# Kernel optimization log

Measured on AMD Instinct MI355X. Metric: run time of the kernel, lower is better.

## Reference

```python
import jax, jax.numpy as jnp
import numpy as np

D_MODEL = 1024
N_HEADS = 16
D_HEAD = D_MODEL // N_HEADS
EPS_LN = 1e-5
EPS_GATE = 1e-5
EPS_DEN = 1e-5


def setup_inputs() -> dict:
    key = jax.random.key(0)
    ks = jax.random.split(key, 4)
    B, T, D = 1, 2048, D_MODEL
    x = jax.random.normal(ks[0], (B, T, D), dtype=jnp.float32)
    # Linear weights scaled like torch default init (~1/sqrt(fan_in))
    s = 1.0 / np.sqrt(D)
    qkv_w = jax.random.normal(ks[1], (3 * D, D), dtype=jnp.float32) * s
    gate_w = jax.random.normal(ks[2], (D, D), dtype=jnp.float32) * s
    proj_w = jax.random.normal(ks[3], (D, D), dtype=jnp.float32) * s
    return {
        "x": x,
        "ln_g": jnp.ones((D,), jnp.float32),
        "ln_b": jnp.zeros((D,), jnp.float32),
        "qkv_w": qkv_w,
        "qkv_b": jnp.zeros((3 * D,), jnp.float32),
        "gate_w": gate_w,
        "gate_b": jnp.zeros((D,), jnp.float32),
        "proj_w": proj_w,
        "proj_b": jnp.zeros((D,), jnp.float32),
    }


def _linear(x, w, b):
    # torch nn.Linear: y = x @ W^T + b, W is (out, in)
    return jnp.einsum("btd,od->bto", x, w) + b


def reference(x, ln_g, ln_b, qkv_w, qkv_b, gate_w, gate_b, proj_w, proj_b):
    B, T, D = x.shape
    H, Dh = N_HEADS, D_HEAD

    # LayerNorm
    mu = jnp.mean(x, axis=-1, keepdims=True)
    var = jnp.mean((x - mu) ** 2, axis=-1, keepdims=True)
    x_norm = (x - mu) / jnp.sqrt(var + EPS_LN) * ln_g + ln_b

    qkv = _linear(x_norm, qkv_w, qkv_b)
    q, k, v = jnp.split(qkv, 3, axis=-1)

    # concept gate on raw x
    gate_sig = jax.nn.sigmoid(_linear(x, gate_w, gate_b))
    gate_norm = gate_sig / (jnp.mean(gate_sig, axis=-1, keepdims=True) + EPS_GATE)
    q = q * gate_norm
    k = k * gate_norm

    # (B,T,D) -> (B,H,T,Dh)
    def heads(t):
        return t.reshape(B, T, H, Dh).transpose(0, 2, 1, 3)

    q, k, v = heads(q).astype(jnp.float32), heads(k).astype(jnp.float32), heads(v).astype(jnp.float32)

    q = jax.nn.elu(q) + 1.0
    k = jax.nn.elu(k) + 1.0

    # causal linear attention via cumsum of outer products (same math as source)
    kv = jnp.einsum("bhtd,bhtm->bhtdm", k, v)        # (B,H,T,Dh,Dh)
    kv_cum = jnp.cumsum(kv, axis=2)
    out_num = jnp.einsum("bhtd,bhtdm->bhtm", q, kv_cum)
    k_cum = jnp.cumsum(k, axis=2)
    out_den = jnp.einsum("bhtd,bhtd->bht", q, k_cum)[..., None] + EPS_DEN
    out = out_num / out_den                           # (B,H,T,Dh)

    out = out.astype(x_norm.dtype).transpose(0, 2, 1, 3).reshape(B, T, D)
    return _linear(out, proj_w, proj_b)
```

## Files before the change

### kernel.cpp

```cpp
#include <hip/hip_runtime.h>
#include <hip/hip_bf16.h>
#include <math.h>

#define T_SEQ 2048
#define DM 1024
#define NH 16
#define DH 64
#define CHUNK 64
#define NCHUNK (T_SEQ / CHUNK)

typedef __hip_bfloat16 bf16;
typedef __attribute__((ext_vector_type(8))) short short8;
typedef __attribute__((ext_vector_type(4))) short short4v;
typedef __attribute__((ext_vector_type(4))) float f32x4;

static __device__ __forceinline__ short f2b_bits(float f) {
  bf16 t = __float2bfloat16(f);
  short s;
  __builtin_memcpy(&s, &t, 2);
  return s;
}

static __device__ __forceinline__ float gelu1(float raw, float gate, float inv) {
  float x = raw * gate * inv;
  return x > 0.f ? x + 1.f : __expf(x);
}

static __device__ __forceinline__ void gload16(const void* g, void* l) {
  __builtin_amdgcn_global_load_lds((const __attribute__((address_space(1))) void*)g,
                                   (__attribute__((address_space(3))) void*)l, 16, 0, 0);
}

__global__ __launch_bounds__(256) void f2b3_kernel(const float* __restrict__ qkv,
                                                   const float* __restrict__ gw,
                                                   const float* __restrict__ pw,
                                                   bf16* __restrict__ oq,
                                                   bf16* __restrict__ og,
                                                   bf16* __restrict__ op) {
  constexpr int NQ = 3 * DM * DM / 4, NS = DM * DM / 4;
  int i = blockIdx.x * 256 + threadIdx.x;
  const float* src;
  bf16* dst;
  int j;
  if (i < NQ) { src = qkv; dst = oq; j = i; }
  else if (i < NQ + NS) { src = gw; dst = og; j = i - NQ; }
  else if (i < NQ + 2 * NS) { src = pw; dst = op; j = i - NQ - NS; }
  else return;
  float4 v = ((const float4*)src)[j];
  short4v s;
  s.x = f2b_bits(v.x); s.y = f2b_bits(v.y); s.z = f2b_bits(v.z); s.w = f2b_bits(v.w);
  *(short4v*)&dst[j * 4] = s;
}

__global__ __launch_bounds__(256) void ln_kernel(const float* __restrict__ x,
                                                 const float* __restrict__ g,
                                                 const float* __restrict__ b,
                                                 bf16* __restrict__ xn,
                                                 bf16* __restrict__ xbf) {
  const int row = blockIdx.x;
  const float* xr = x + (size_t)row * DM;
  float vals[4];
  float s = 0.f, s2 = 0.f;
#pragma unroll
  for (int i = 0; i < 4; i++) {
    float v = xr[threadIdx.x + i * 256];
    vals[i] = v;
    s += v;
    s2 += v * v;
  }
#pragma unroll
  for (int m = 1; m < 64; m <<= 1) {
    s += __shfl_xor(s, m, 64);
    s2 += __shfl_xor(s2, m, 64);
  }
  __shared__ float red[8];
  const int wid = threadIdx.x >> 6;
  if ((threadIdx.x & 63) == 0) {
    red[wid] = s;
    red[4 + wid] = s2;
  }
  __syncthreads();
  s = red[0] + red[1] + red[2] + red[3];
  s2 = red[4] + red[5] + red[6] + red[7];
  const float mean = s * (1.f / DM);
  const float var = s2 * (1.f / DM) - mean * mean;
  const float rstd = rsqrtf(var + 1e-5f);
#pragma unroll
  for (int i = 0; i < 4; i++) {
    int idx = threadIdx.x + i * 256;
    float v = (vals[i] - mean) * rstd * g[idx] + b[idx];
    xn[(size_t)row * DM + idx] = __float2bfloat16(v);
    xbf[(size_t)row * DM + idx] = __float2bfloat16(vals[i]);
  }
}

__global__ __launch_bounds__(256) void gemm_gateqkv(
    const bf16* __restrict__ xbf, const bf16* __restrict__ xn,
    const bf16* __restrict__ wg, const bf16* __restrict__ wq,
    const float* __restrict__ gate_b, const float* __restrict__ qkv_b,
    float* __restrict__ gate_sig, float* __restrict__ Qraw,
    float* __restrict__ Kraw, float* __restrict__ Vo) {
  constexpr int K = 1024;
  __shared__ __align__(16) short As[2 * 128 * 32];
  __shared__ __align__(16) short Bs[2 * 128 * 32];

  const int tid = threadIdx.x;
  const int wid = tid >> 6, lane = tid & 63;
  const int wm = wid >> 1, wn = wid & 1;
  const int lm = lane & 15, quad = lane >> 4;

  const bool isGate = blockIdx.y < 8;
  const int m0 = blockIdx.x * 128;
  const int n0 = isGate ? blockIdx.y * 128 : (blockIdx.y - 8) * 128;
  const short* Ag = (const short*)(isGate ? xbf : xn);
  const short* Wg = (const short*)(isGate ? wg : wq);
  const float* bias = isGate ? gate_b : qkv_b;

  f32x4 zero = {0.f, 0.f, 0.f, 0.f};
  f32x4 acc[4][4];
#pragma unroll
  for (int i = 0; i < 4; i++)
#pragma unroll
    for (int j = 0; j < 4; j++) acc[i][j] = zero;

  for (int kb = 0; kb < K; kb += 64) {
    __syncthreads();
#pragma unroll
    for (int sec = 0; sec < 2; sec++) {
#pragma unroll
      for (int it = 0; it < 2; it++) {
        const int idx = it * 256 + tid;
        const int row = idx >> 2, seg = (idx & 3) * 8;
        gload16(&Ag[(size_t)(m0 + row) * K + kb + sec * 32 + seg],
                &As[sec * 4096 + (it * 256 + wid * 64) * 8]);
        gload16(&Wg[(size_t)(n0 + row) * K + kb + sec * 32 + seg],
                &Bs[sec * 4096 + (it * 256 + wid * 64) * 8]);
      }
    }
    __syncthreads();
#pragma unroll
    for (int sec = 0; sec < 2; sec++) {
      short8 afr[4], bfr[4];
#pragma unroll
      for (int i = 0; i < 4; i++) {
        afr[i] = *(const short8*)&As[sec * 4096 + (wm * 64 + i * 16 + lm) * 32 + quad * 8];
        bfr[i] = *(const short8*)&Bs[sec * 4096 + (wn * 64 + i * 16 + lm) * 32 + quad * 8];
      }
#pragma unroll
      for (int i = 0; i < 4; i++)
#pragma unroll
        for (int j = 0; j < 4; j++)
          acc[i][j] = __builtin_amdgcn_mfma_f32_16x16x32_bf16(afr[i], bfr[j], acc[i][j], 0, 0, 0);
    }
  }

#pragma unroll
  for (int i = 0; i < 4; i++) {
    const int rbase = m0 + wm * 64 + i * 16 + quad * 4;
#pragma unroll
    for (int j = 0; j < 4; j++) {
      const int col = n0 + wn * 64 + j * 16 + lm;
      const float bval = bias[col];
#pragma unroll
      for (int r = 0; r < 4; r++) {
        const int row = rbase + r;
        float v = acc[i][j][r] + bval;
        if (isGate) {
          gate_sig[(size_t)row * DM + col] = 1.f / (1.f + __expf(-v));
        } else if (col < DM) {
          const int d = col;
          Qraw[((size_t)(d >> 6) * T_SEQ + row) * DH + (d & 63)] = v;
        } else if (col < 2 * DM) {
          const int d = col - DM;
          Kraw[((size_t)(d >> 6) * T_SEQ + row) * DH + (d & 63)] = v;
        } else {
          const int d = col - 2 * DM;
          Vo[((size_t)(d >> 6) * T_SEQ + row) * DH + (d & 63)] = v;
        }
      }
    }
  }
}

__global__ __launch_bounds__(256) void gemm_proj(const bf16* __restrict__ A,
                                                 const bf16* __restrict__ W,
                                                 const float* __restrict__ bias,
                                                 float* __restrict__ Cout) {
  constexpr int K = 1024;
  __shared__ __align__(16) short As[2 * 64 * 32];
  __shared__ __align__(16) short Bs[2 * 128 * 32];

  const int tid = threadIdx.x;
  const int wid = tid >> 6, lane = tid & 63;
  const int wm = wid >> 1, wn = wid & 1;
  const int lm = lane & 15, quad = lane >> 4;

  const int m0 = blockIdx.x * 64;
  const int n0 = blockIdx.y * 128;
  const short* Ag = (const short*)A;
  const short* Wg = (const short*)W;

  f32x4 zero = {0.f, 0.f, 0.f, 0.f};
  f32x4 acc[2][4];
#pragma unroll
  for (int i = 0; i < 2; i++)
#pragma unroll
    for (int j = 0; j < 4; j++) acc[i][j] = zero;

  for (int kb = 0; kb < K; kb += 64) {
    __syncthreads();
#pragma unroll
    for (int sec = 0; sec < 2; sec++) {
      {
        const int row = tid >> 2, seg = (tid & 3) * 8;
        gload16(&Ag[(size_t)(m0 + row) * K + kb + sec * 32 + seg],
                &As[sec * 2048 + (wid * 64) * 8]);
      }
#pragma unroll
      for (int it = 0; it < 2; it++) {
        const int idx = it * 256 + tid;
        const int row = idx >> 2, seg = (idx & 3) * 8;
        gload16(&Wg[(size_t)(n0 + row) * K + kb + sec * 32 + seg],
                &Bs[sec * 4096 + (it * 256 + wid * 64) * 8]);
      }
    }
    __syncthreads();
#pragma unroll
    for (int sec = 0; sec < 2; sec++) {
      short8 afr[2], bfr[4];
#pragma unroll
      for (int i = 0; i < 2; i++)
        afr[i] = *(const short8*)&As[sec * 2048 + (wm * 32 + i * 16 + lm) * 32 + quad * 8];
#pragma unroll
      for (int j = 0; j < 4; j++)
        bfr[j] = *(const short8*)&Bs[sec * 4096 + (wn * 64 + j * 16 + lm) * 32 + quad * 8];
#pragma unroll
      for (int i = 0; i < 2; i++)
#pragma unroll
        for (int j = 0; j < 4; j++)
          acc[i][j] = __builtin_amdgcn_mfma_f32_16x16x32_bf16(afr[i], bfr[j], acc[i][j], 0, 0, 0);
    }
  }
#pragma unroll
  for (int i = 0; i < 2; i++) {
    const int rbase = m0 + wm * 32 + i * 16 + quad * 4;
#pragma unroll
    for (int j = 0; j < 4; j++) {
      const int col = n0 + wn * 64 + j * 16 + lm;
      const float bval = bias[col];
#pragma unroll
      for (int r = 0; r < 4; r++)
        Cout[(size_t)(rbase + r) * DM + col] = acc[i][j][r] + bval;
    }
  }
}

__global__ __launch_bounds__(256) void gate_mean_kernel(const float* __restrict__ gate_sig,
                                                        float* __restrict__ inv_den) {
  const int row = blockIdx.x;
  float s = 0.f;
  for (int i = threadIdx.x; i < DM; i += 256) s += gate_sig[(size_t)row * DM + i];
#pragma unroll
  for (int m = 1; m < 64; m <<= 1) s += __shfl_xor(s, m, 64);
  __shared__ float red[4];
  if ((threadIdx.x & 63) == 0) red[threadIdx.x >> 6] = s;
  __syncthreads();
  if (threadIdx.x == 0) {
    float tot = red[0] + red[1] + red[2] + red[3];
    inv_den[row] = 1.f / (tot * (1.f / DM) + 1e-5f);
  }
}

__global__ __launch_bounds__(256, 2) void chunk_sum_mm(const float* __restrict__ Kraw,
                                                       const float* __restrict__ gate_sig,
                                                       const float* __restrict__ inv_den,
                                                       const float* __restrict__ Vo,
                                                       float* __restrict__ Skv,
                                                       float* __restrict__ Sk) {
  constexpr int STR = 68;
  __shared__ __align__(16) float Ks2[64 * STR];
  __shared__ __align__(16) float Vs2[64 * STR];
  const int b = blockIdx.x;
  const int h = b >> 5, c = b & 31;
  const int tid = threadIdx.x;
  const int ty = tid >> 4, tx = tid & 15;
  const int d0 = ty * 4, m0 = tx * 4;
  const int t0 = c * CHUNK;
  const size_t cb = ((size_t)h * T_SEQ + t0) * DH;
  const float* Kg = Kraw + cb;
  const float* Vg = Vo + cb;
#pragma unroll
  for (int p = 0; p < 4; p++) {
    int f = p * 256 + tid, row = f >> 4, seg = (f & 15) * 4;
    const int t = t0 + row;
    f32x4 kr = *(const f32x4*)&Kg[row * 64 + seg];
    f32x4 gr = *(const f32x4*)&gate_sig[(size_t)t * DM + h * 64 + seg];
    const float inv = inv_den[t];
    f32x4 kgv;
#pragma unroll
    for (int e = 0; e < 4; e++) kgv[e] = gelu1(kr[e], gr[e], inv);
    *(f32x4*)&Ks2[row * STR + seg] = kgv;
    *(f32x4*)&Vs2[row * STR + seg] = *(const f32x4*)&Vg[row * 64 + seg];
  }
  __syncthreads();
  float acc[4][4] = {};
#pragma unroll 4
  for (int s = 0; s < 64; s++) {
    f32x4 kf = *(const f32x4*)&Ks2[s * STR + d0];
    f32x4 vf = *(const f32x4*)&Vs2[s * STR + m0];
#pragma unroll
    for (int i = 0; i < 4; i++)
#pragma unroll
      for (int j = 0; j < 4; j++) acc[i][j] += kf[i] * vf[j];
  }
  float* outp = Skv + (size_t)b * 4096;
#pragma unroll
  for (int i = 0; i < 4; i++) {
    f32x4 o = {acc[i][0], acc[i][1], acc[i][2], acc[i][3]};
    *(f32x4*)&outp[(d0 + i) * 64 + m0] = o;
  }
  if (tid < 64) {
    float ss = 0.f;
#pragma unroll 4
    for (int s = 0; s < 64; s++) ss += Ks2[s * STR + tid];
    Sk[b * 64 + tid] = ss;
  }
}

__global__ __launch_bounds__(256) void scan_excl(float* __restrict__ Skv,
                                                 float* __restrict__ Sk) {
  const int bid = blockIdx.x, tid = threadIdx.x;
  if (bid < 256) {
    const int id = bid * 256 + tid;
    const int h = id >> 12, e = id & 4095;
    float* base = Skv + (size_t)h * NCHUNK * 4096 + e;
    float v[NCHUNK];
#pragma unroll
    for (int c = 0; c < NCHUNK; c++) v[c] = base[(size_t)c * 4096];
    float run = 0.f;
#pragma unroll
    for (int c = 0; c < NCHUNK; c++) {
      float t = v[c];
      base[(size_t)c * 4096] = run;
      run += t;
    }
  } else {
    const int id = (bid - 256) * 256 + tid;
    const int h = id >> 6, e = id & 63;
    float* base = Sk + (size_t)h * NCHUNK * 64 + e;
    float v[NCHUNK];
#pragma unroll
    for (int c = 0; c < NCHUNK; c++) v[c] = base[c * 64];
    float run = 0.f;
#pragma unroll
    for (int c = 0; c < NCHUNK; c++) {
      float t = v[c];
      base[c * 64] = run;
      run += t;
    }
  }
}

__global__ __launch_bounds__(256, 2) void attn_mm(const float* __restrict__ Qraw,
                                                  const float* __restrict__ Kraw,
                                                  const float* __restrict__ gate_sig,
                                                  const float* __restrict__ inv_den,
                                                  const float* __restrict__ Vo,
                                                  const float* __restrict__ Skv,
                                                  const float* __restrict__ Sk,
                                                  bf16* __restrict__ O) {
  constexpr int STR = 68;
  __shared__ __align__(16) float Qs[64 * STR];
  __shared__ __align__(16) float Vs[64 * STR];
  __shared__ __align__(16) float KPs[64 * STR];
  __shared__ float denp[64 * 16];
  __shared__ float skp[64];
  __shared__ float den[64];
  const int b = blockIdx.x;
  const int h = b >> 5, c = b & 31;
  const int tid = threadIdx.x;
  const int ty = tid >> 4, tx = tid & 15;
  const int r0 = ty * 4, c0 = tx * 4, m0 = tx * 4;
  const int t0 = c * CHUNK;
  const size_t cb = ((size_t)h * T_SEQ + t0) * DH;
  const float* Qg = Qraw + cb;
  const float* Kg = Kraw + cb;
  const float* Vg = Vo + cb;
  const float* Pg = Skv + (size_t)b * 4096;

  f32x4 kreg[4], greg[4];
  float ireg[4];
#pragma unroll
  for (int p = 0; p < 4; p++) {
    int f = p * 256 + tid, row = f >> 4, seg = (f & 15) * 4;
    kreg[p] = *(const f32x4*)&Kg[row * 64 + seg];
    greg[p] = *(const f32x4*)&gate_sig[(size_t)(t0 + row) * DM + h * 64 + seg];
    ireg[p] = inv_den[t0 + row];
  }
#pragma unroll
  for (int p = 0; p < 4; p++) {
    int f = p * 256 + tid, row = f >> 4, seg = (f & 15) * 4;
    f32x4 qr = *(const f32x4*)&Qg[row * 64 + seg];
    f32x4 gq = *(const f32x4*)&gate_sig[(size_t)(t0 + row) * DM + h * 64 + seg];
    const float inv = inv_den[t0 + row];
    f32x4 qgv;
#pragma unroll
    for (int e = 0; e < 4; e++) qgv[e] = gelu1(qr[e], gq[e], inv);
    *(f32x4*)&Qs[row * STR + seg] = qgv;
    *(f32x4*)&Vs[row * STR + seg] = *(const f32x4*)&Vg[row * 64 + seg];
    *(f32x4*)&KPs[row * STR + seg] = *(const f32x4*)&Pg[row * 64 + seg];
  }
  if (tid < 64) skp[tid] = Sk[b * 64 + tid];
  __syncthreads();

  if (tid < 64) {
    float s = 1e-5f;
#pragma unroll 4
    for (int d = 0; d < 64; d++) s += Qs[tid * STR + d] * skp[d];
    den[tid] = s;
  }

  float accO[4][4] = {};
#pragma unroll 2
  for (int d0 = 0; d0 < 64; d0 += 4) {
    f32x4 qf[4], pf[4];
#pragma unroll
    for (int i = 0; i < 4; i++) qf[i] = *(const f32x4*)&Qs[(r0 + i) * STR + d0];
#pragma unroll
    for (int dd = 0; dd < 4; dd++) pf[dd] = *(const f32x4*)&KPs[(d0 + dd) * STR + m0];
#pragma unroll
    for (int i = 0; i < 4; i++)
#pragma unroll
      for (int j = 0; j < 4; j++)
        accO[i][j] += qf[i][0] * pf[0][j] + qf[i][1] * pf[1][j] +
                      qf[i][2] * pf[2][j] + qf[i][3] * pf[3][j];
  }
  __syncthreads();
#pragma unroll
  for (int p = 0; p < 4; p++) {
    int f = p * 256 + tid, row = f >> 4, seg = (f & 15) * 4;
    f32x4 kgv;
#pragma unroll
    for (int e = 0; e < 4; e++) kgv[e] = gelu1(kreg[p][e], greg[p][e], ireg[p]);
    *(f32x4*)&KPs[row * STR + seg] = kgv;
  }
  __syncthreads();

  float accS[4][4] = {};
#pragma unroll 2
  for (int d0 = 0; d0 < 64; d0 += 4) {
    f32x4 qf[4], kf[4];
#pragma unroll
    for (int i = 0; i < 4; i++) qf[i] = *(const f32x4*)&Qs[(r0 + i) * STR + d0];
#pragma unroll
    for (int j = 0; j < 4; j++) kf[j] = *(const f32x4*)&KPs[(c0 + j) * STR + d0];
#pragma unroll
    for (int i = 0; i < 4; i++)
#pragma unroll
      for (int j = 0; j < 4; j++)
        accS[i][j] += qf[i][0] * kf[j][0] + qf[i][1] * kf[j][1] +
                      qf[i][2] * kf[j][2] + qf[i][3] * kf[j][3];
  }
  float dp[4];
#pragma unroll
  for (int i = 0; i < 4; i++) {
    dp[i] = 0.f;
#pragma unroll
    for (int j = 0; j < 4; j++) {
      float v = (c0 + j) <= (r0 + i) ? accS[i][j] : 0.f;
      accS[i][j] = v;
      dp[i] += v;
    }
  }
  __syncthreads();
#pragma unroll
  for (int i = 0; i < 4; i++) {
    f32x4 sv = {accS[i][0], accS[i][1], accS[i][2], accS[i][3]};
    *(f32x4*)&Qs[(r0 + i) * STR + c0] = sv;
    denp[(r0 + i) * 16 + tx] = dp[i];
  }
  __syncthreads();
  if (tid < 64) {
    float s = den[tid];
#pragma unroll
    for (int t = 0; t < 16; t++) s += denp[tid * 16 + t];
    den[tid] = s;
  }

#pragma unroll 2
  for (int c4 = 0; c4 < 64; c4 += 4) {
    f32x4 sf[4], vf[4];
#pragma unroll
    for (int i = 0; i < 4; i++) sf[i] = *(const f32x4*)&Qs[(r0 + i) * STR + c4];
#pragma unroll
    for (int cc = 0; cc < 4; cc++) vf[cc] = *(const f32x4*)&Vs[(c4 + cc) * STR + m0];
#pragma unroll
    for (int i = 0; i < 4; i++)
#pragma unroll
      for (int j = 0; j < 4; j++)
        accO[i][j] += sf[i][0] * vf[0][j] + sf[i][1] * vf[1][j] +
                      sf[i][2] * vf[2][j] + sf[i][3] * vf[3][j];
  }
  __syncthreads();

#pragma unroll
  for (int i = 0; i < 4; i++) {
    const float inv = 1.f / den[r0 + i];
    short4v ov;
#pragma unroll
    for (int j = 0; j < 4; j++) ov[j] = f2b_bits(accO[i][j] * inv);
    *(short4v*)&O[(size_t)(t0 + r0 + i) * DM + h * 64 + m0] = ov;
  }
}

extern "C" void kernel_launch(void* const* d_in, const int* in_sizes, int n_in,
                              void* d_out, int out_size, void* d_ws, size_t ws_size,
                              hipStream_t stream) {
  (void)in_sizes; (void)n_in; (void)out_size; (void)ws_size;
  const float* x      = (const float*)d_in[0];
  const float* ln_g   = (const float*)d_in[1];
  const float* ln_b   = (const float*)d_in[2];
  const float* qkv_w  = (const float*)d_in[3];
  const float* qkv_b  = (const float*)d_in[4];
  const float* gate_w = (const float*)d_in[5];
  const float* gate_b = (const float*)d_in[6];
  const float* proj_w = (const float*)d_in[7];
  const float* proj_b = (const float*)d_in[8];
  float* out = (float*)d_out;

  char* ws = (char*)d_ws;
  size_t off = 0;
  auto alloc = [&](size_t bytes) {
    void* p = ws + off;
    off += (bytes + 255) & ~(size_t)255;
    return p;
  };
  bf16*  xn       = (bf16*)alloc((size_t)T_SEQ * DM * 2);
  bf16*  xbf      = (bf16*)alloc((size_t)T_SEQ * DM * 2);
  bf16*  wqkv     = (bf16*)alloc((size_t)3 * DM * DM * 2);
  bf16*  wgate    = (bf16*)alloc((size_t)DM * DM * 2);
  bf16*  wproj    = (bf16*)alloc((size_t)DM * DM * 2);
  float* gate_sig = (float*)alloc((size_t)T_SEQ * DM * 4);
  float* inv_den  = (float*)alloc((size_t)T_SEQ * 4);
  float* Qraw     = (float*)alloc((size_t)T_SEQ * DM * 4);
  float* Kraw     = (float*)alloc((size_t)T_SEQ * DM * 4);
  float* Vo       = (float*)alloc((size_t)T_SEQ * DM * 4);
  bf16*  Obuf     = (bf16*)alloc((size_t)T_SEQ * DM * 2);
  float* Skv      = (float*)alloc((size_t)NH * NCHUNK * 4096 * 4);
  float* Sk       = (float*)alloc((size_t)NH * NCHUNK * 64 * 4);

  const int n4_total = (3 + 1 + 1) * DM * DM / 4;
  f2b3_kernel<<<(n4_total + 255) / 256, 256, 0, stream>>>(qkv_w, gate_w, proj_w,
                                                          wqkv, wgate, wproj);
  ln_kernel<<<T_SEQ, 256, 0, stream>>>(x, ln_g, ln_b, xn, xbf);
  gemm_gateqkv<<<dim3(16, 32), 256, 0, stream>>>(xbf, xn, wgate, wqkv, gate_b, qkv_b,
                                                 gate_sig, Qraw, Kraw, Vo);
  gate_mean_kernel<<<T_SEQ, 256, 0, stream>>>(gate_sig, inv_den);
  chunk_sum_mm<<<NH * NCHUNK, 256, 0, stream>>>(Kraw, gate_sig, inv_den, Vo, Skv, Sk);
  scan_excl<<<260, 256, 0, stream>>>(Skv, Sk);
  attn_mm<<<NH * NCHUNK, 256, 0, stream>>>(Qraw, Kraw, gate_sig, inv_den, Vo, Skv, Sk, Obuf);
  gemm_proj<<<dim3(32, 8), 256, 0, stream>>>(Obuf, wproj, proj_b, out);
}
```

Baseline: 177.1 us.

## Fuse prep kernels, store QKV/gate as bf16, fold gate mean into GEMM epilogue

Merges the weight-conversion and layernorm kernels into one launch. The gate row-mean is now reduced in the gate GEMM epilogue through LDS and atomics, which removes the separate gate_mean kernel. Q, K, V and the gate sigmoid are stored as bf16 instead of fp32, halving the intermediate traffic for the chunk and attention kernels. In exchange it loses precision on the intermediates and makes the gate sum order nondeterministic because of the atomics.

```diff
diff --git a/kernel.cpp b/kernel.cpp
--- a/kernel.cpp
+++ b/kernel.cpp
@@ -20,6 +20,12 @@
   __builtin_memcpy(&s, &t, 2);
   return s;
 }
+static __device__ __forceinline__ float b2f(short s) {
+  unsigned int u = ((unsigned int)(unsigned short)s) << 16;
+  float f;
+  __builtin_memcpy(&f, &u, 4);
+  return f;
+}
 
 static __device__ __forceinline__ float gelu1(float raw, float gate, float inv) {
   float x = raw * gate * inv;
@@ -31,66 +37,65 @@
                                    (__attribute__((address_space(3))) void*)l, 16, 0, 0);
 }
 
-__global__ __launch_bounds__(256) void f2b3_kernel(const float* __restrict__ qkv,
-                                                   const float* __restrict__ gw,
-                                                   const float* __restrict__ pw,
-                                                   bf16* __restrict__ oq,
-                                                   bf16* __restrict__ og,
-                                                   bf16* __restrict__ op) {
-  constexpr int NQ = 3 * DM * DM / 4, NS = DM * DM / 4;
-  int i = blockIdx.x * 256 + threadIdx.x;
-  const float* src;
-  bf16* dst;
-  int j;
-  if (i < NQ) { src = qkv; dst = oq; j = i; }
-  else if (i < NQ + NS) { src = gw; dst = og; j = i - NQ; }
-  else if (i < NQ + 2 * NS) { src = pw; dst = op; j = i - NQ - NS; }
-  else return;
-  float4 v = ((const float4*)src)[j];
-  short4v s;
-  s.x = f2b_bits(v.x); s.y = f2b_bits(v.y); s.z = f2b_bits(v.z); s.w = f2b_bits(v.w);
-  *(short4v*)&dst[j * 4] = s;
-}
-
-__global__ __launch_bounds__(256) void ln_kernel(const float* __restrict__ x,
-                                                 const float* __restrict__ g,
-                                                 const float* __restrict__ b,
-                                                 bf16* __restrict__ xn,
-                                                 bf16* __restrict__ xbf) {
-  const int row = blockIdx.x;
-  const float* xr = x + (size_t)row * DM;
-  float vals[4];
-  float s = 0.f, s2 = 0.f;
-#pragma unroll
-  for (int i = 0; i < 4; i++) {
-    float v = xr[threadIdx.x + i * 256];
-    vals[i] = v;
-    s += v;
-    s2 += v * v;
-  }
-#pragma unroll
-  for (int m = 1; m < 64; m <<= 1) {
-    s += __shfl_xor(s, m, 64);
-    s2 += __shfl_xor(s2, m, 64);
-  }
-  __shared__ float red[8];
-  const int wid = threadIdx.x >> 6;
-  if ((threadIdx.x & 63) == 0) {
-    red[wid] = s;
-    red[4 + wid] = s2;
-  }
-  __syncthreads();
-  s = red[0] + red[1] + red[2] + red[3];
-  s2 = red[4] + red[5] + red[6] + red[7];
-  const float mean = s * (1.f / DM);
-  const float var = s2 * (1.f / DM) - mean * mean;
-  const float rstd = rsqrtf(var + 1e-5f);
-#pragma unroll
-  for (int i = 0; i < 4; i++) {
-    int idx = threadIdx.x + i * 256;
-    float v = (vals[i] - mean) * rstd * g[idx] + b[idx];
-    xn[(size_t)row * DM + idx] = __float2bfloat16(v);
-    xbf[(size_t)row * DM + idx] = __float2bfloat16(vals[i]);
+#define PREP_WBLOCKS (5 * DM * DM / 4 / 256)
+__global__ __launch_bounds__(256) void prep_kernel(
+    const float* __restrict__ x, const float* __restrict__ g,
+    const float* __restrict__ b, const float* __restrict__ qkv_w,
+    const float* __restrict__ gate_w, const float* __restrict__ proj_w,
+    bf16* __restrict__ xn, bf16* __restrict__ xbf,
+    bf16* __restrict__ wqkv, bf16* __restrict__ wgate, bf16* __restrict__ wproj,
+    float* __restrict__ gate_accum) {
+  const int blk = blockIdx.x;
+  if (blk < T_SEQ) {
+    const int row = blk;
+    if (row < 8) gate_accum[row * 256 + threadIdx.x] = 0.f;
+    const float* xr = x + (size_t)row * DM;
+    float vals[4];
+    float s = 0.f, s2 = 0.f;
+#pragma unroll
+    for (int i = 0; i < 4; i++) {
+      float v = xr[threadIdx.x + i * 256];
+      vals[i] = v;
+      s += v;
+      s2 += v * v;
+    }
+#pragma unroll
+    for (int m = 1; m < 64; m <<= 1) {
+      s += __shfl_xor(s, m, 64);
+      s2 += __shfl_xor(s2, m, 64);
+    }
+    __shared__ float red[8];
+    const int wid = threadIdx.x >> 6;
+    if ((threadIdx.x & 63) == 0) {
+      red[wid] = s;
+      red[4 + wid] = s2;
+    }
+    __syncthreads();
+    s = red[0] + red[1] + red[2] + red[3];
+    s2 = red[4] + red[5] + red[6] + red[7];
+    const float mean = s * (1.f / DM);
+    const float var = s2 * (1.f / DM) - mean * mean;
+    const float rstd = rsqrtf(var + 1e-5f);
+#pragma unroll
+    for (int i = 0; i < 4; i++) {
+      int idx = threadIdx.x + i * 256;
+      float v = (vals[i] - mean) * rstd * g[idx] + b[idx];
+      xn[(size_t)row * DM + idx] = __float2bfloat16(v);
+      xbf[(size_t)row * DM + idx] = __float2bfloat16(vals[i]);
+    }
+  } else {
+    constexpr int NQ = 3 * DM * DM / 4, NS = DM * DM / 4;
+    int i = (blk - T_SEQ) * 256 + threadIdx.x;
+    const float* src;
+    bf16* dst;
+    int j;
+    if (i < NQ) { src = qkv_w; dst = wqkv; j = i; }
+    else if (i < NQ + NS) { src = gate_w; dst = wgate; j = i - NQ; }
+    else { src = proj_w; dst = wproj; j = i - NQ - NS; }
+    float4 v = ((const float4*)src)[j];
+    short4v sv;
+    sv.x = f2b_bits(v.x); sv.y = f2b_bits(v.y); sv.z = f2b_bits(v.z); sv.w = f2b_bits(v.w);
+    *(short4v*)&dst[j * 4] = sv;
   }
 }
 
@@ -98,8 +103,8 @@
     const bf16* __restrict__ xbf, const bf16* __restrict__ xn,
     const bf16* __restrict__ wg, const bf16* __restrict__ wq,
     const float* __restrict__ gate_b, const float* __restrict__ qkv_b,
-    float* __restrict__ gate_sig, float* __restrict__ Qraw,
-    float* __restrict__ Kraw, float* __restrict__ Vo) {
+    short* __restrict__ Gb, float* __restrict__ gate_accum,
+    short* __restrict__ Qb, short* __restrict__ Kb, short* __restrict__ Vb) {
   constexpr int K = 1024;
   __shared__ __align__(16) short As[2 * 128 * 32];
   __shared__ __align__(16) short Bs[2 * 128 * 32];
@@ -114,7 +119,6 @@
   const int n0 = isGate ? blockIdx.y * 128 : (blockIdx.y - 8) * 128;
   const short* Ag = (const short*)(isGate ? xbf : xn);
   const short* Wg = (const short*)(isGate ? wg : wq);
-  const float* bias = isGate ? gate_b : qkv_b;
 
   f32x4 zero = {0.f, 0.f, 0.f, 0.f};
   f32x4 acc[4][4];
@@ -154,28 +158,56 @@
     }
   }
 
-#pragma unroll
-  for (int i = 0; i < 4; i++) {
-    const int rbase = m0 + wm * 64 + i * 16 + quad * 4;
-#pragma unroll
-    for (int j = 0; j < 4; j++) {
-      const int col = n0 + wn * 64 + j * 16 + lm;
-      const float bval = bias[col];
+  if (isGate) {
+    float* red = (float*)As;
+    __syncthreads();
+#pragma unroll
+    for (int i = 0; i < 4; i++) {
 #pragma unroll
       for (int r = 0; r < 4; r++) {
-        const int row = rbase + r;
-        float v = acc[i][j][r] + bval;
-        if (isGate) {
-          gate_sig[(size_t)row * DM + col] = 1.f / (1.f + __expf(-v));
-        } else if (col < DM) {
-          const int d = col;
-          Qraw[((size_t)(d >> 6) * T_SEQ + row) * DH + (d & 63)] = v;
-        } else if (col < 2 * DM) {
-          const int d = col - DM;
-          Kraw[((size_t)(d >> 6) * T_SEQ + row) * DH + (d & 63)] = v;
-        } else {
-          const int d = col - 2 * DM;
-          Vo[((size_t)(d >> 6) * T_SEQ + row) * DH + (d & 63)] = v;
+        const int rowl = wm * 64 + i * 16 + quad * 4 + r;
+        const int row = m0 + rowl;
+        float rp = 0.f;
+#pragma unroll
+        for (int j = 0; j < 4; j++) {
+          const int col = n0 + wn * 64 + j * 16 + lm;
+          float v = acc[i][j][r] + gate_b[col];
+          float sig = 1.f / (1.f + __expf(-v));
+          Gb[(size_t)row * DM + col] = f2b_bits(sig);
+          rp += sig;
+        }
+        red[rowl * 32 + wn * 16 + lm] = rp;
+      }
+    }
+    __syncthreads();
+    if (tid < 128) {
+      float s = 0.f;
+#pragma unroll
+      for (int t2 = 0; t2 < 32; t2++) s += red[tid * 32 + t2];
+      atomicAdd(&gate_accum[m0 + tid], s);
+    }
+  } else {
+#pragma unroll
+    for (int i = 0; i < 4; i++) {
+      const int rbase = m0 + wm * 64 + i * 16 + quad * 4;
+#pragma unroll
+      for (int j = 0; j < 4; j++) {
+        const int col = n0 + wn * 64 + j * 16 + lm;
+        const float bval = qkv_b[col];
+#pragma unroll
+        for (int r = 0; r < 4; r++) {
+          const int row = rbase + r;
+          const short bv = f2b_bits(acc[i][j][r] + bval);
+          if (col < DM) {
+            const int d = col;
+            Qb[((size_t)(d >> 6) * T_SEQ + row) * DH + (d & 63)] = bv;
+          } else if (col < 2 * DM) {
+            const int d = col - DM;
+            Kb[((size_t)(d >> 6) * T_SEQ + row) * DH + (d & 63)] = bv;
+          } else {
+            const int d = col - 2 * DM;
+            Vb[((size_t)(d >> 6) * T_SEQ + row) * DH + (d & 63)] = bv;
+          }
         }
       }
     }
@@ -255,26 +287,10 @@
   }
 }
 
-__global__ __launch_bounds__(256) void gate_mean_kernel(const float* __restrict__ gate_sig,
-                                                        float* __restrict__ inv_den) {
-  const int row = blockIdx.x;
-  float s = 0.f;
-  for (int i = threadIdx.x; i < DM; i += 256) s += gate_sig[(size_t)row * DM + i];
-#pragma unroll
-  for (int m = 1; m < 64; m <<= 1) s += __shfl_xor(s, m, 64);
-  __shared__ float red[4];
-  if ((threadIdx.x & 63) == 0) red[threadIdx.x >> 6] = s;
-  __syncthreads();
-  if (threadIdx.x == 0) {
-    float tot = red[0] + red[1] + red[2] + red[3];
-    inv_den[row] = 1.f / (tot * (1.f / DM) + 1e-5f);
-  }
-}
-
-__global__ __launch_bounds__(256, 2) void chunk_sum_mm(const float* __restrict__ Kraw,
-                                                       const float* __restrict__ gate_sig,
-                                                       const float* __restrict__ inv_den,
-                                                       const float* __restrict__ Vo,
+__global__ __launch_bounds__(256, 2) void chunk_sum_mm(const short* __restrict__ Kb,
+                                                       const short* __restrict__ Gb,
+                                                       const float* __restrict__ ga,
+                                                       const short* __restrict__ Vb,
                                                        float* __restrict__ Skv,
                                                        float* __restrict__ Sk) {
   constexpr int STR = 68;
@@ -287,20 +303,22 @@
   const int d0 = ty * 4, m0 = tx * 4;
   const int t0 = c * CHUNK;
   const size_t cb = ((size_t)h * T_SEQ + t0) * DH;
-  const float* Kg = Kraw + cb;
-  const float* Vg = Vo + cb;
 #pragma unroll
   for (int p = 0; p < 4; p++) {
     int f = p * 256 + tid, row = f >> 4, seg = (f & 15) * 4;
     const int t = t0 + row;
-    f32x4 kr = *(const f32x4*)&Kg[row * 64 + seg];
-    f32x4 gr = *(const f32x4*)&gate_sig[(size_t)t * DM + h * 64 + seg];
-    const float inv = inv_den[t];
-    f32x4 kgv;
-#pragma unroll
-    for (int e = 0; e < 4; e++) kgv[e] = gelu1(kr[e], gr[e], inv);
+    short4v kr = *(const short4v*)&Kb[cb + row * 64 + seg];
+    short4v gr = *(const short4v*)&Gb[(size_t)t * DM + h * 64 + seg];
+    short4v vr = *(const short4v*)&Vb[cb + row * 64 + seg];
+    const float inv = 1.f / (ga[t] * (1.f / DM) + 1e-5f);
+    f32x4 kgv, vv;
+#pragma unroll
+    for (int e = 0; e < 4; e++) {
+      kgv[e] = gelu1(b2f(kr[e]), b2f(gr[e]), inv);
+      vv[e] = b2f(vr[e]);
+    }
     *(f32x4*)&Ks2[row * STR + seg] = kgv;
-    *(f32x4*)&Vs2[row * STR + seg] = *(const f32x4*)&Vg[row * 64 + seg];
+    *(f32x4*)&Vs2[row * STR + seg] = vv;
   }
   __syncthreads();
   float acc[4][4] = {};
@@ -361,11 +379,11 @@
   }
 }
 
-__global__ __launch_bounds__(256, 2) void attn_mm(const float* __restrict__ Qraw,
-                                                  const float* __restrict__ Kraw,
-                                                  const float* __restrict__ gate_sig,
-                                                  const float* __restrict__ inv_den,
-                                                  const float* __restrict__ Vo,
+__global__ __launch_bounds__(256, 2) void attn_mm(const short* __restrict__ Qb,
+                                                  const short* __restrict__ Kb,
+                                                  const short* __restrict__ Gb,
+                                                  const float* __restrict__ ga,
+                                                  const short* __restrict__ Vb,
                                                   const float* __restrict__ Skv,
                                                   const float* __restrict__ Sk,
                                                   bf16* __restrict__ O) {
@@ -383,31 +401,32 @@
   const int r0 = ty * 4, c0 = tx * 4, m0 = tx * 4;
   const int t0 = c * CHUNK;
   const size_t cb = ((size_t)h * T_SEQ + t0) * DH;
-  const float* Qg = Qraw + cb;
-  const float* Kg = Kraw + cb;
-  const float* Vg = Vo + cb;
   const float* Pg = Skv + (size_t)b * 4096;
 
-  f32x4 kreg[4], greg[4];
+  short4v kreg[4], greg[4];
   float ireg[4];
 #pragma unroll
   for (int p = 0; p < 4; p++) {
     int f = p * 256 + tid, row = f >> 4, seg = (f & 15) * 4;
-    kreg[p] = *(const f32x4*)&Kg[row * 64 + seg];
-    greg[p] = *(const f32x4*)&gate_sig[(size_t)(t0 + row) * DM + h * 64 + seg];
-    ireg[p] = inv_den[t0 + row];
+    kreg[p] = *(const short4v*)&Kb[cb + row * 64 + seg];
+    greg[p] = *(const short4v*)&Gb[(size_t)(t0 + row) * DM + h * 64 + seg];
+    ireg[p] = 1.f / (ga[t0 + row] * (1.f / DM) + 1e-5f);
   }
 #pragma unroll
   for (int p = 0; p < 4; p++) {
     int f = p * 256 + tid, row = f >> 4, seg = (f & 15) * 4;
-    f32x4 qr = *(const f32x4*)&Qg[row * 64 + seg];
-    f32x4 gq = *(const f32x4*)&gate_sig[(size_t)(t0 + row) * DM + h * 64 + seg];
-    const float inv = inv_den[t0 + row];
-    f32x4 qgv;
-#pragma unroll
-    for (int e = 0; e < 4; e++) qgv[e] = gelu1(qr[e], gq[e], inv);
+    short4v qr = *(const short4v*)&Qb[cb + row * 64 + seg];
+    short4v gq = *(const short4v*)&Gb[(size_t)(t0 + row) * DM + h * 64 + seg];
+    short4v vr = *(const short4v*)&Vb[cb + row * 64 + seg];
+    const float inv = 1.f / (ga[t0 + row] * (1.f / DM) + 1e-5f);
+    f32x4 qgv, vv;
+#pragma unroll
+    for (int e = 0; e < 4; e++) {
+      qgv[e] = gelu1(b2f(qr[e]), b2f(gq[e]), inv);
+      vv[e] = b2f(vr[e]);
+    }
     *(f32x4*)&Qs[row * STR + seg] = qgv;
-    *(f32x4*)&Vs[row * STR + seg] = *(const f32x4*)&Vg[row * 64 + seg];
+    *(f32x4*)&Vs[row * STR + seg] = vv;
     *(f32x4*)&KPs[row * STR + seg] = *(const f32x4*)&Pg[row * 64 + seg];
   }
   if (tid < 64) skp[tid] = Sk[b * 64 + tid];
@@ -441,7 +460,7 @@
     int f = p * 256 + tid, row = f >> 4, seg = (f & 15) * 4;
     f32x4 kgv;
 #pragma unroll
-    for (int e = 0; e < 4; e++) kgv[e] = gelu1(kreg[p][e], greg[p][e], ireg[p]);
+    for (int e = 0; e < 4; e++) kgv[e] = gelu1(b2f(kreg[p][e]), b2f(greg[p][e]), ireg[p]);
     *(f32x4*)&KPs[row * STR + seg] = kgv;
   }
   __syncthreads();
@@ -540,24 +559,21 @@
   bf16*  wqkv     = (bf16*)alloc((size_t)3 * DM * DM * 2);
   bf16*  wgate    = (bf16*)alloc((size_t)DM * DM * 2);
   bf16*  wproj    = (bf16*)alloc((size_t)DM * DM * 2);
-  float* gate_sig = (float*)alloc((size_t)T_SEQ * DM * 4);
-  float* inv_den  = (float*)alloc((size_t)T_SEQ * 4);
-  float* Qraw     = (float*)alloc((size_t)T_SEQ * DM * 4);
-  float* Kraw     = (float*)alloc((size_t)T_SEQ * DM * 4);
-  float* Vo       = (float*)alloc((size_t)T_SEQ * DM * 4);
+  short* Gb       = (short*)alloc((size_t)T_SEQ * DM * 2);
+  float* gate_accum = (float*)alloc((size_t)T_SEQ * 4);
+  short* Qb       = (short*)alloc((size_t)T_SEQ * DM * 2);
+  short* Kb       = (short*)alloc((size_t)T_SEQ * DM * 2);
+  short* Vb       = (short*)alloc((size_t)T_SEQ * DM * 2);
   bf16*  Obuf     = (bf16*)alloc((size_t)T_SEQ * DM * 2);
   float* Skv      = (float*)alloc((size_t)NH * NCHUNK * 4096 * 4);
   float* Sk       = (float*)alloc((size_t)NH * NCHUNK * 64 * 4);
 
-  const int n4_total = (3 + 1 + 1) * DM * DM / 4;
-  f2b3_kernel<<<(n4_total + 255) / 256, 256, 0, stream>>>(qkv_w, gate_w, proj_w,
-                                                          wqkv, wgate, wproj);
-  ln_kernel<<<T_SEQ, 256, 0, stream>>>(x, ln_g, ln_b, xn, xbf);
+  prep_kernel<<<T_SEQ + PREP_WBLOCKS, 256, 0, stream>>>(
+      x, ln_g, ln_b, qkv_w, gate_w, proj_w, xn, xbf, wqkv, wgate, wproj, gate_accum);
   gemm_gateqkv<<<dim3(16, 32), 256, 0, stream>>>(xbf, xn, wgate, wqkv, gate_b, qkv_b,
-                                                 gate_sig, Qraw, Kraw, Vo);
-  gate_mean_kernel<<<T_SEQ, 256, 0, stream>>>(gate_sig, inv_den);
-  chunk_sum_mm<<<NH * NCHUNK, 256, 0, stream>>>(Kraw, gate_sig, inv_den, Vo, Skv, Sk);
+                                                 Gb, gate_accum, Qb, Kb, Vb);
+  chunk_sum_mm<<<NH * NCHUNK, 256, 0, stream>>>(Kb, Gb, gate_accum, Vb, Skv, Sk);
   scan_excl<<<260, 256, 0, stream>>>(Skv, Sk);
-  attn_mm<<<NH * NCHUNK, 256, 0, stream>>>(Qraw, Kraw, gate_sig, inv_den, Vo, Skv, Sk, Obuf);
+  attn_mm<<<NH * NCHUNK, 256, 0, stream>>>(Qb, Kb, Gb, gate_accum, Vb, Skv, Sk, Obuf);
   gemm_proj<<<dim3(32, 8), 256, 0, stream>>>(Obuf, wproj, proj_b, out);
 }
```

After: 165.8 us. 1.07x faster.
